# Kernel optimization log

Hardware: AMD Instinct MI355X
Metric: run time of the kernel (lower is better)

The kernel has to match this reference:

```python
import jax, jax.numpy as jnp
import numpy as np

B, L, C = 4, 16384, 512   # batch, tokens (128x128 grid), dim
NH, WS = 8, 8             # num_heads, window grid (ws)
HD = C // NH              # head_dim = 64


def setup_inputs() -> dict:
    key = jax.random.key(0)
    k1, k2, k3, k4, k5 = jax.random.split(key, 5)
    return {
        "q":   jax.random.normal(k1, (B, L, C), dtype=jnp.float32),
        "kv":  jax.random.normal(k2, (B, L, C), dtype=jnp.float32),
        "Wq":  jax.random.normal(k3, (C, C), dtype=jnp.float32) * 0.02,
        "Wkv": jax.random.normal(k4, (C, 2 * C), dtype=jnp.float32) * 0.02,
        "Wfc": jax.random.normal(k5, (C, C), dtype=jnp.float32) * 0.02,
    }


def reference(q, kv, Wq, Wkv, Wfc):
    Bq, Lq, Cd = q.shape
    Lkv = kv.shape[1]
    nh, hd, ws = NH, Cd // NH, WS
    scale = hd ** (-0.5)
    hw_q = int(round(Lq ** 0.5))   # 128
    hw_k = int(round(Lkv ** 0.5))
    sq, sk = hw_q // ws, hw_k // ws  # window side lengths (16)

    qp = q @ Wq                                   # [B, Lq, C]
    kvp = (kv @ Wkv).reshape(Bq, Lkv, 2, Cd)
    k, v = kvp[:, :, 0], kvp[:, :, 1]             # [B, Lkv, C]

    def window(x, s):
        # [B, hw, hw, C] -> [B, ws*ws windows, heads, s*s tokens, hd]
        x = x.reshape(Bq, ws, s, ws, s, Cd).transpose(0, 1, 3, 2, 4, 5)
        x = x.reshape(Bq, ws * ws, s * s, nh, hd)
        return x.transpose(0, 1, 3, 2, 4)

    qw = window(qp, sq)   # [B, W, H, sq*sq, hd]
    kw = window(k, sk)    # [B, W, H, sk*sk, hd]
    vw = window(v, sk)

    attn = jnp.einsum('bwhqd,bwhkd->bwhqk', qw, kw) * scale
    attn = jax.nn.softmax(attn, axis=-1)
    o = jnp.einsum('bwhqk,bwhkd->bwhqd', attn, vw)  # [B, W, H, sq*sq, hd]

    # inverse window partition
    o = o.transpose(0, 1, 3, 2, 4).reshape(Bq, ws, ws, sq, sq, Cd)
    o = o.transpose(0, 1, 3, 2, 4, 5).reshape(Bq, Lq, Cd)
    return o @ Wfc
```

## Files before the change

kernel.cpp:

```cpp
#include <hip/hip_runtime.h>
#include <stdint.h>

#define BB 4
#define LL 16384
#define CC 512
#define MM (BB * LL)

typedef unsigned short u16;
typedef __bf16 bf16x8 __attribute__((ext_vector_type(8)));
typedef float f32x4 __attribute__((ext_vector_type(4)));
typedef u16 u16x8 __attribute__((ext_vector_type(8)));
typedef u16 u16x4 __attribute__((ext_vector_type(4)));

__device__ __forceinline__ u16 f2bf(float f) {
  return __builtin_bit_cast(u16, (__bf16)f);
}

__device__ __forceinline__ void gl_lds16(const void* g, void* l) {
  __builtin_amdgcn_global_load_lds((const __attribute__((address_space(1))) void*)g,
                                   (__attribute__((address_space(3))) void*)l,
                                   16, 0, 0);
}

__global__ void cvt2_kernel(const float* __restrict__ q, const float* __restrict__ kv,
                            u16* __restrict__ qo, u16* __restrict__ kvo, int n4) {
  for (int i = blockIdx.x * blockDim.x + threadIdx.x; i < 2 * n4; i += gridDim.x * blockDim.x) {
    const float* src = (i < n4) ? q : kv;
    u16* dst = (i < n4) ? qo : kvo;
    int k = (i < n4) ? i : i - n4;
    float4 v = reinterpret_cast<const float4*>(src)[k];
    u16x4 o;
    o[0] = f2bf(v.x); o[1] = f2bf(v.y); o[2] = f2bf(v.z); o[3] = f2bf(v.w);
    reinterpret_cast<u16x4*>(dst)[k] = o;
  }
}

__global__ void tcvt3_kernel(const float* __restrict__ Wq, const float* __restrict__ Wkv,
                             const float* __restrict__ Wfc, u16* __restrict__ Wq_t,
                             u16* __restrict__ Wkv_t, u16* __restrict__ Wfc_t) {
  int idx = blockIdx.x * blockDim.x + threadIdx.x;
  const float* W; u16* Wt; int N, li;
  if (idx < 262144)      { W = Wq;  Wt = Wq_t;  N = 512;  li = idx; }
  else if (idx < 786432) { W = Wkv; Wt = Wkv_t; N = 1024; li = idx - 262144; }
  else                   { W = Wfc; Wt = Wfc_t; N = 512;  li = idx - 786432; }
  int n = li / 512, k = li % 512;
  Wt[li] = f2bf(W[k * N + n]);
}

template <bool OUT_F32>
__global__ __launch_bounds__(512, 2) void gemm256(const u16* __restrict__ A,
                                                  const u16* __restrict__ Bt,
                                                  void* __restrict__ Cp,
                                                  int M, int N, int K) {
  __shared__ __align__(16) u16 Al[2][16384];
  __shared__ __align__(16) u16 Bl[2][16384];
  const int nbn = N >> 8;
  const int nwg = gridDim.x;
  const int bid0 = blockIdx.x;
  const int cpx = nwg >> 3;
  const int bid = (bid0 & 7) * cpx + (bid0 >> 3);
  const int bm = bid / nbn, bn = bid % nbn;
  const size_t row0 = (size_t)bm << 8, col0 = (size_t)bn << 8;
  const int tid = threadIdx.x, lane = tid & 63;
  const int wv = tid >> 6, wm = wv >> 2, wn = wv & 3;
  const int ro = lane & 15, g4 = lane >> 4;
  const int NT = K >> 6;

  const int ci0 = tid, ci1 = tid + 512;
  const int r0 = ci0 >> 3, g0 = (ci0 & 7) ^ (r0 & 7);
  const int r1 = ci1 >> 3, g1 = (ci1 & 7) ^ (r1 & 7);

  auto stageA = [&](int half, int kt, u16* L) {
    gl_lds16(A + (row0 + half * 128 + r0) * (size_t)K + kt * 64 + g0 * 8, L + half * 8192 + ci0 * 8);
    gl_lds16(A + (row0 + half * 128 + r1) * (size_t)K + kt * 64 + g1 * 8, L + half * 8192 + ci1 * 8);
  };
  auto stageB = [&](int half, int kt, u16* L) {
    gl_lds16(Bt + (col0 + half * 128 + r0) * (size_t)K + kt * 64 + g0 * 8, L + half * 8192 + ci0 * 8);
    gl_lds16(Bt + (col0 + half * 128 + r1) * (size_t)K + kt * 64 + g1 * 8, L + half * 8192 + ci1 * 8);
  };

  const int aB = (wm * 128 + ro) * 64;
  const int bB = (wn * 64 + ro) * 64;
  const int sw0 = (g4 ^ (ro & 7)) * 8;
  const int sw1 = ((g4 + 4) ^ (ro & 7)) * 8;

  auto ldf = [&](const u16* p) { return *reinterpret_cast<const bf16x8*>(p); };

  f32x4 acc[8][4] = {};

  stageA(0, 0, Al[0]); stageA(1, 0, Al[0]); stageB(0, 0, Bl[0]); stageB(1, 0, Bl[0]);
  stageB(0, 1, Bl[1]); stageB(1, 1, Bl[1]);
  asm volatile("s_waitcnt vmcnt(4)" ::: "memory");
  __builtin_amdgcn_s_barrier();

  for (int t = 0; t < NT; t += 2) {
#pragma unroll
    for (int half = 0; half < 2; ++half) {
      const int u = t + half;
      u16* LA = Al[half];
      u16* LB = Bl[half];
      u16* LAn = Al[half ^ 1];
      const bool stA = (u + 1) < NT;
      const bool stB = (u + 2) < NT;
      bf16x8 bfr[4][2], af[2][2];

#pragma unroll
      for (int n = 0; n < 4; ++n) {
        bfr[n][0] = ldf(LB + bB + n * 1024 + sw0);
        bfr[n][1] = ldf(LB + bB + n * 1024 + sw1);
      }
      af[0][0] = ldf(LA + aB + sw0);        af[0][1] = ldf(LA + aB + sw1);
      af[1][0] = ldf(LA + aB + 1024 + sw0); af[1][1] = ldf(LA + aB + 1024 + sw1);
      if (stA) stageA(0, u + 1, LAn);
      __builtin_amdgcn_s_barrier();
      asm volatile("s_waitcnt lgkmcnt(0)" ::: "memory");
      __builtin_amdgcn_sched_barrier(0);
      __builtin_amdgcn_s_setprio(1);
#pragma unroll
      for (int m = 0; m < 2; ++m)
#pragma unroll
        for (int n = 0; n < 4; ++n) {
          acc[m][n] = __builtin_amdgcn_mfma_f32_16x16x32_bf16(af[m][0], bfr[n][0], acc[m][n], 0, 0, 0);
          acc[m][n] = __builtin_amdgcn_mfma_f32_16x16x32_bf16(af[m][1], bfr[n][1], acc[m][n], 0, 0, 0);
        }
      __builtin_amdgcn_s_setprio(0);
      __builtin_amdgcn_s_barrier();

#pragma unroll
      for (int ph = 1; ph < 4; ++ph) {
        af[0][0] = ldf(LA + aB + (2 * ph) * 1024 + sw0);
        af[0][1] = ldf(LA + aB + (2 * ph) * 1024 + sw1);
        af[1][0] = ldf(LA + aB + (2 * ph + 1) * 1024 + sw0);
        af[1][1] = ldf(LA + aB + (2 * ph + 1) * 1024 + sw1);
        if (ph == 1) { if (stA) stageA(1, u + 1, LAn); }
        else if (ph == 2) { if (stB) stageB(0, u + 2, LB); }
        else { if (stB) stageB(1, u + 2, LB); }
        __builtin_amdgcn_s_barrier();
        asm volatile("s_waitcnt lgkmcnt(0)" ::: "memory");
        __builtin_amdgcn_sched_barrier(0);
        __builtin_amdgcn_s_setprio(1);
#pragma unroll
        for (int m = 0; m < 2; ++m)
#pragma unroll
          for (int n = 0; n < 4; ++n) {
            acc[2 * ph + m][n] =
                __builtin_amdgcn_mfma_f32_16x16x32_bf16(af[m][0], bfr[n][0], acc[2 * ph + m][n], 0, 0, 0);
            acc[2 * ph + m][n] =
                __builtin_amdgcn_mfma_f32_16x16x32_bf16(af[m][1], bfr[n][1], acc[2 * ph + m][n], 0, 0, 0);
          }
        __builtin_amdgcn_s_setprio(0);
        if (ph == 3) {
          if (stB) asm volatile("s_waitcnt vmcnt(4)" ::: "memory");
          else     asm volatile("s_waitcnt vmcnt(0)" ::: "memory");
        }
        __builtin_amdgcn_s_barrier();
      }
    }
  }

#pragma unroll
  for (int m = 0; m < 8; ++m)
#pragma unroll
    for (int n = 0; n < 4; ++n)
#pragma unroll
      for (int j = 0; j < 4; ++j) {
        size_t r = row0 + wm * 128 + m * 16 + g4 * 4 + j;
        size_t c = col0 + wn * 64 + n * 16 + ro;
        if (OUT_F32)
          reinterpret_cast<float*>(Cp)[r * N + c] = acc[m][n][j];
        else
          reinterpret_cast<u16*>(Cp)[r * N + c] = f2bf(acc[m][n][j]);
      }
}

__global__ __launch_bounds__(512, 4) void attn_kernel(const u16* __restrict__ qp,
                                                      const u16* __restrict__ kvp,
                                                      u16* __restrict__ o) {
  __shared__ __align__(16) u16 Kl[256 * 64];
  __shared__ __align__(16) u16 Vt[64 * 256];
  __shared__ __align__(16) u16 Pl[8 * 1024];
  const int bid = blockIdx.x;
  const int h = bid & 7, w = (bid >> 3) & 63, b = bid >> 9;
  const int w1 = w >> 3, w2 = w & 7;
  const int tid = threadIdx.x, lane = tid & 63, wv = tid >> 6;

  auto lrow = [&](int t) { return (w1 * 16 + (t >> 4)) * 128 + w2 * 16 + (t & 15); };

#pragma unroll
  for (int p = 0; p < 4; ++p) {
    int ci = tid + p * 512;
    int r = ci >> 3, g = (ci & 7) ^ (r & 7);
    gl_lds16(kvp + ((size_t)(b * LL + lrow(r))) * 1024 + h * 64 + g * 8, Kl + ci * 8);
  }
  {
    const int tk = tid >> 1, half = tid & 1;
    const size_t base = ((size_t)(b * LL + lrow(tk))) * 1024 + 512 + h * 64 + half * 32;
#pragma unroll
    for (int c = 0; c < 4; ++c) {
      u16x8 vx = *reinterpret_cast<const u16x8*>(kvp + base + c * 8);
#pragma unroll
      for (int e = 0; e < 8; ++e) {
        int d = half * 32 + c * 8 + e;
        Vt[d * 256 + (((tk >> 3) ^ (d & 7)) * 8) + (tk & 7)] = vx[e];
      }
    }
  }
  __syncthreads();

  const int ro = lane & 15;
  const int g4 = lane >> 4;
  const float scale = 0.125f;
  const int swA = (g4 ^ (ro & 7)) * 8;
  const int swB = ((g4 + 4) ^ (ro & 7)) * 8;
  u16* PW = Pl + wv * 1024;

  auto ldf = [&](const u16* p) { return *reinterpret_cast<const bf16x8*>(p); };

#pragma unroll
  for (int rt = 0; rt < 2; ++rt) {
    const int tq = 32 * wv + 16 * rt + ro;
    const size_t qbase = ((size_t)(b * LL + lrow(tq))) * 512 + h * 64 + g4 * 8;
    const bf16x8 qf0 = *reinterpret_cast<const bf16x8*>(qp + qbase);
    const bf16x8 qf1 = *reinterpret_cast<const bf16x8*>(qp + qbase + 32);

    f32x4 sa[16] = {};
    __builtin_amdgcn_s_setprio(1);
#pragma unroll
    for (int ct = 0; ct < 16; ++ct) {
      bf16x8 kf0 = ldf(Kl + (16 * ct + ro) * 64 + swA);
      bf16x8 kf1 = ldf(Kl + (16 * ct + ro) * 64 + swB);
      sa[ct] = __builtin_amdgcn_mfma_f32_16x16x32_bf16(qf0, kf0, sa[ct], 0, 0, 0);
      sa[ct] = __builtin_amdgcn_mfma_f32_16x16x32_bf16(qf1, kf1, sa[ct], 0, 0, 0);
    }
    __builtin_amdgcn_s_setprio(0);

#pragma unroll
    for (int j = 0; j < 4; ++j) {
      float m = -1e30f;
#pragma unroll
      for (int ct = 0; ct < 16; ++ct) m = fmaxf(m, sa[ct][j]);
      m = fmaxf(m, __shfl_xor(m, 1));
      m = fmaxf(m, __shfl_xor(m, 2));
      m = fmaxf(m, __shfl_xor(m, 4));
      m = fmaxf(m, __shfl_xor(m, 8));
      m *= scale;
      float s = 0.f;
#pragma unroll
      for (int ct = 0; ct < 16; ++ct) {
        float p = __expf(sa[ct][j] * scale - m);
        sa[ct][j] = p;
        s += p;
      }
      s += __shfl_xor(s, 1);
      s += __shfl_xor(s, 2);
      s += __shfl_xor(s, 4);
      s += __shfl_xor(s, 8);
      float inv = 1.f / s;
#pragma unroll
      for (int ct = 0; ct < 16; ++ct) sa[ct][j] *= inv;
    }

    f32x4 oacc[4] = {};
#pragma unroll
    for (int kh = 0; kh < 4; ++kh) {
#pragma unroll
      for (int c = 0; c < 4; ++c)
#pragma unroll
        for (int j = 0; j < 4; ++j) {
          int rq = g4 * 4 + j;
          PW[rq * 64 + (((2 * c + (ro >> 3)) ^ (rq & 7)) * 8) + (ro & 7)] =
              f2bf(sa[kh * 4 + c][j]);
        }
      __builtin_amdgcn_s_setprio(1);
#pragma unroll
      for (int ks = 0; ks < 2; ++ks) {
        bf16x8 pf = ldf(PW + ro * 64 + (((ks * 4 + g4) ^ (ro & 7)) * 8));
        const int kkg = kh * 2 + ks;
#pragma unroll
        for (int cd = 0; cd < 4; ++cd) {
          bf16x8 vf = ldf(Vt + (16 * cd + ro) * 256 + (((kkg * 4 + g4) ^ (ro & 7)) * 8));
          oacc[cd] = __builtin_amdgcn_mfma_f32_16x16x32_bf16(pf, vf, oacc[cd], 0, 0, 0);
        }
      }
      __builtin_amdgcn_s_setprio(0);
    }

#pragma unroll
    for (int cd = 0; cd < 4; ++cd)
#pragma unroll
      for (int j = 0; j < 4; ++j) {
        int t = 32 * wv + 16 * rt + g4 * 4 + j;
        int d = 16 * cd + ro;
        o[((size_t)(b * LL + lrow(t))) * 512 + h * 64 + d] = f2bf(oacc[cd][j]);
      }
  }
}

extern "C" void kernel_launch(void* const* d_in, const int* in_sizes, int n_in,
                              void* d_out, int out_size, void* d_ws, size_t ws_size,
                              hipStream_t stream) {
  const float* q = (const float*)d_in[0];
  const float* kv = (const float*)d_in[1];
  const float* Wq = (const float*)d_in[2];
  const float* Wkv = (const float*)d_in[3];
  const float* Wfc = (const float*)d_in[4];
  float* out = (float*)d_out;
  char* ws = (char*)d_ws;

  u16* q_bf  = (u16*)(ws + 0);
  u16* kv_bf = (u16*)(ws + 67108864);
  u16* qp    = (u16*)(ws + 134217728);
  u16* kvp   = (u16*)(ws + 201326592);
  u16* Wq_t  = (u16*)(ws + 335544320);
  u16* Wkv_t = (u16*)(ws + 336068608);
  u16* Wfc_t = (u16*)(ws + 337117184);
  u16* o_buf = q_bf;

  const int n4 = MM * CC / 4;
  cvt2_kernel<<<4096, 256, 0, stream>>>(q, kv, q_bf, kv_bf, n4);
  tcvt3_kernel<<<4096, 256, 0, stream>>>(Wq, Wkv, Wfc, Wq_t, Wkv_t, Wfc_t);

  gemm256<false><<<(MM / 256) * (CC / 256), 512, 0, stream>>>(q_bf, Wq_t, qp, MM, CC, CC);
  gemm256<false><<<(MM / 256) * (2 * CC / 256), 512, 0, stream>>>(kv_bf, Wkv_t, kvp, MM, 2 * CC, CC);

  attn_kernel<<<BB * 64 * 8, 512, 0, stream>>>(qp, kvp, o_buf);

  gemm256<true><<<(MM / 256) * (CC / 256), 512, 0, stream>>>(o_buf, Wfc_t, out, MM, CC, CC);
}
```

Before: 371.0 us.

## Fuse fp32-to-bf16 activation conversion into the projection GEMM A-tile load

Removes the separate cvt2 kernel that converted q and kv to bf16. The projection GEMMs now read fp32 activations straight into registers, convert them to bf16, and write them to LDS with the same swizzle, with the register prefetch overlapped across the pipeline phases. This saves a full write and re-read of two 64 MB bf16 buffers. In exchange, the GEMM A path reads twice the bytes, loses the async global-to-LDS load, uses more registers, and inserts a vmcnt(0) wait mid-iteration. The kv GEMM re-reads its fp32 A tile for each of its four column blocks.

Measured after the change: 383.9 us. 3.5% more time.

```diff
diff --git a/kernel.cpp b/kernel.cpp
--- a/kernel.cpp
+++ b/kernel.cpp
@@ -20,19 +20,6 @@
   __builtin_amdgcn_global_load_lds((const __attribute__((address_space(1))) void*)g,
                                    (__attribute__((address_space(3))) void*)l,
                                    16, 0, 0);
-}
-
-__global__ void cvt2_kernel(const float* __restrict__ q, const float* __restrict__ kv,
-                            u16* __restrict__ qo, u16* __restrict__ kvo, int n4) {
-  for (int i = blockIdx.x * blockDim.x + threadIdx.x; i < 2 * n4; i += gridDim.x * blockDim.x) {
-    const float* src = (i < n4) ? q : kv;
-    u16* dst = (i < n4) ? qo : kvo;
-    int k = (i < n4) ? i : i - n4;
-    float4 v = reinterpret_cast<const float4*>(src)[k];
-    u16x4 o;
-    o[0] = f2bf(v.x); o[1] = f2bf(v.y); o[2] = f2bf(v.z); o[3] = f2bf(v.w);
-    reinterpret_cast<u16x4*>(dst)[k] = o;
-  }
 }
 
 __global__ void tcvt3_kernel(const float* __restrict__ Wq, const float* __restrict__ Wkv,
@@ -47,8 +34,8 @@
   Wt[li] = f2bf(W[k * N + n]);
 }
 
-template <bool OUT_F32>
-__global__ __launch_bounds__(512, 2) void gemm256(const u16* __restrict__ A,
+template <bool A_F32, bool OUT_F32>
+__global__ __launch_bounds__(512, 2) void gemm256(const void* __restrict__ Ap,
                                                   const u16* __restrict__ Bt,
                                                   void* __restrict__ Cp,
                                                   int M, int N, int K) {
@@ -66,17 +53,41 @@
   const int ro = lane & 15, g4 = lane >> 4;
   const int NT = K >> 6;
 
-  const int ci0 = tid, ci1 = tid + 512;
-  const int r0 = ci0 >> 3, g0 = (ci0 & 7) ^ (r0 & 7);
-  const int r1 = ci1 >> 3, g1 = (ci1 & 7) ^ (r1 & 7);
-
-  auto stageA = [&](int half, int kt, u16* L) {
-    gl_lds16(A + (row0 + half * 128 + r0) * (size_t)K + kt * 64 + g0 * 8, L + half * 8192 + ci0 * 8);
-    gl_lds16(A + (row0 + half * 128 + r1) * (size_t)K + kt * 64 + g1 * 8, L + half * 8192 + ci1 * 8);
+  const u16* A16 = (const u16*)Ap;
+  const float* A32 = (const float*)Ap;
+
+  const int cis[4] = {tid, tid + 512, tid + 1024, tid + 1536};
+  int crs[4], cgs[4];
+#pragma unroll
+  for (int c = 0; c < 4; ++c) { crs[c] = cis[c] >> 3; cgs[c] = (cis[c] & 7) ^ (crs[c] & 7); }
+  const int r0 = crs[0], g0 = cgs[0], r1 = crs[1], g1 = cgs[1];
+
+  auto stageA16 = [&](int half, int kt, u16* L) {
+    gl_lds16(A16 + (row0 + half * 128 + r0) * (size_t)K + kt * 64 + g0 * 8, L + half * 8192 + tid * 8);
+    gl_lds16(A16 + (row0 + half * 128 + r1) * (size_t)K + kt * 64 + g1 * 8, L + half * 8192 + (tid + 512) * 8);
   };
   auto stageB = [&](int half, int kt, u16* L) {
-    gl_lds16(Bt + (col0 + half * 128 + r0) * (size_t)K + kt * 64 + g0 * 8, L + half * 8192 + ci0 * 8);
-    gl_lds16(Bt + (col0 + half * 128 + r1) * (size_t)K + kt * 64 + g1 * 8, L + half * 8192 + ci1 * 8);
+    gl_lds16(Bt + (col0 + half * 128 + r0) * (size_t)K + kt * 64 + g0 * 8, L + half * 8192 + tid * 8);
+    gl_lds16(Bt + (col0 + half * 128 + r1) * (size_t)K + kt * 64 + g1 * 8, L + half * 8192 + (tid + 512) * 8);
+  };
+
+  f32x4 av[4][2];
+  auto aload = [&](int kt) {
+#pragma unroll
+    for (int c = 0; c < 4; ++c) {
+      const float* s = A32 + (row0 + crs[c]) * (size_t)K + kt * 64 + cgs[c] * 8;
+      av[c][0] = *reinterpret_cast<const f32x4*>(s);
+      av[c][1] = *reinterpret_cast<const f32x4*>(s + 4);
+    }
+  };
+  auto awrite = [&](u16* L) {
+#pragma unroll
+    for (int c = 0; c < 4; ++c) {
+      bf16x8 wq;
+#pragma unroll
+      for (int e = 0; e < 8; ++e) wq[e] = (__bf16)av[c][e >> 2][e & 3];
+      *reinterpret_cast<bf16x8*>(L + cis[c] * 8) = wq;
+    }
   };
 
   const int aB = (wm * 128 + ro) * 64;
@@ -88,9 +99,18 @@
 
   f32x4 acc[8][4] = {};
 
-  stageA(0, 0, Al[0]); stageA(1, 0, Al[0]); stageB(0, 0, Bl[0]); stageB(1, 0, Bl[0]);
-  stageB(0, 1, Bl[1]); stageB(1, 1, Bl[1]);
-  asm volatile("s_waitcnt vmcnt(4)" ::: "memory");
+  if (A_F32) {
+    aload(0);
+    stageB(0, 0, Bl[0]); stageB(1, 0, Bl[0]);
+    stageB(0, 1, Bl[1]); stageB(1, 1, Bl[1]);
+    asm volatile("s_waitcnt vmcnt(4)" ::: "memory");
+    awrite(Al[0]);
+    asm volatile("s_waitcnt lgkmcnt(0)" ::: "memory");
+  } else {
+    stageA16(0, 0, Al[0]); stageA16(1, 0, Al[0]); stageB(0, 0, Bl[0]); stageB(1, 0, Bl[0]);
+    stageB(0, 1, Bl[1]); stageB(1, 1, Bl[1]);
+    asm volatile("s_waitcnt vmcnt(4)" ::: "memory");
+  }
   __builtin_amdgcn_s_barrier();
 
   for (int t = 0; t < NT; t += 2) {
@@ -104,6 +124,7 @@
       const bool stB = (u + 2) < NT;
       bf16x8 bfr[4][2], af[2][2];
 
+      if (A_F32) { if (stA) aload(u + 1); }
 #pragma unroll
       for (int n = 0; n < 4; ++n) {
         bfr[n][0] = ldf(LB + bB + n * 1024 + sw0);
@@ -111,7 +132,7 @@
       }
       af[0][0] = ldf(LA + aB + sw0);        af[0][1] = ldf(LA + aB + sw1);
       af[1][0] = ldf(LA + aB + 1024 + sw0); af[1][1] = ldf(LA + aB + 1024 + sw1);
-      if (stA) stageA(0, u + 1, LAn);
+      if (!A_F32) { if (stA) stageA16(0, u + 1, LAn); }
       __builtin_amdgcn_s_barrier();
       asm volatile("s_waitcnt lgkmcnt(0)" ::: "memory");
       __builtin_amdgcn_sched_barrier(0);
@@ -132,9 +153,19 @@
         af[0][1] = ldf(LA + aB + (2 * ph) * 1024 + sw1);
         af[1][0] = ldf(LA + aB + (2 * ph + 1) * 1024 + sw0);
         af[1][1] = ldf(LA + aB + (2 * ph + 1) * 1024 + sw1);
-        if (ph == 1) { if (stA) stageA(1, u + 1, LAn); }
-        else if (ph == 2) { if (stB) stageB(0, u + 2, LB); }
-        else { if (stB) stageB(1, u + 2, LB); }
+        if (A_F32) {
+          if (ph == 2) {
+            asm volatile("s_waitcnt vmcnt(0)" ::: "memory");
+            if (stA) awrite(LAn);
+            if (stB) stageB(0, u + 2, LB);
+          } else if (ph == 3) {
+            if (stB) stageB(1, u + 2, LB);
+          }
+        } else {
+          if (ph == 1) { if (stA) stageA16(1, u + 1, LAn); }
+          else if (ph == 2) { if (stB) stageB(0, u + 2, LB); }
+          else { if (stB) stageB(1, u + 2, LB); }
+        }
         __builtin_amdgcn_s_barrier();
         asm volatile("s_waitcnt lgkmcnt(0)" ::: "memory");
         __builtin_amdgcn_sched_barrier(0);
@@ -149,7 +180,7 @@
                 __builtin_amdgcn_mfma_f32_16x16x32_bf16(af[m][1], bfr[n][1], acc[2 * ph + m][n], 0, 0, 0);
           }
         __builtin_amdgcn_s_setprio(0);
-        if (ph == 3) {
+        if (!A_F32 && ph == 3) {
           if (stB) asm volatile("s_waitcnt vmcnt(4)" ::: "memory");
           else     asm volatile("s_waitcnt vmcnt(0)" ::: "memory");
         }
@@ -307,23 +338,19 @@
   float* out = (float*)d_out;
   char* ws = (char*)d_ws;
 
-  u16* q_bf  = (u16*)(ws + 0);
-  u16* kv_bf = (u16*)(ws + 67108864);
+  u16* o_buf = (u16*)(ws + 0);
   u16* qp    = (u16*)(ws + 134217728);
   u16* kvp   = (u16*)(ws + 201326592);
   u16* Wq_t  = (u16*)(ws + 335544320);
   u16* Wkv_t = (u16*)(ws + 336068608);
   u16* Wfc_t = (u16*)(ws + 337117184);
-  u16* o_buf = q_bf;
-
-  const int n4 = MM * CC / 4;
-  cvt2_kernel<<<4096, 256, 0, stream>>>(q, kv, q_bf, kv_bf, n4);
+
   tcvt3_kernel<<<4096, 256, 0, stream>>>(Wq, Wkv, Wfc, Wq_t, Wkv_t, Wfc_t);
 
-  gemm256<false><<<(MM / 256) * (CC / 256), 512, 0, stream>>>(q_bf, Wq_t, qp, MM, CC, CC);
-  gemm256<false><<<(MM / 256) * (2 * CC / 256), 512, 0, stream>>>(kv_bf, Wkv_t, kvp, MM, 2 * CC, CC);
+  gemm256<true, false><<<(MM / 256) * (CC / 256), 512, 0, stream>>>(q, Wq_t, qp, MM, CC, CC);
+  gemm256<true, false><<<(MM / 256) * (2 * CC / 256), 512, 0, stream>>>(kv, Wkv_t, kvp, MM, 2 * CC, CC);
 
   attn_kernel<<<BB * 64 * 8, 512, 0, stream>>>(qp, kvp, o_buf);
 
-  gemm256<true><<<(MM / 256) * (CC / 256), 512, 0, stream>>>(o_buf, Wfc_t, out, MM, CC, CC);
-}
+  gemm256<false, true><<<(MM / 256) * (CC / 256), 512, 0, stream>>>(o_buf, Wfc_t, out, MM, CC, CC);
+}
```
